# Kernel optimization log

Hardware: AMD Instinct MI355X
Metric: run time of the kernel (lower is better)

The kernel has to match this reference:

```python
import jax, jax.numpy as jnp
import numpy as np
from jax import lax

C_OUT = 32   # out_capsules[0]
D_OUT = 8    # out_capsules[1]
ROUTING_ITERS = 3
EPS = 1e-8


def squash(s):
    # squash over capsule-channel axis c (dim 1 of B c d h w)
    n2 = jnp.sum(s * s, axis=1, keepdims=True)
    return s * (n2 / (1.0 + n2)) / jnp.sqrt(n2 + EPS)


def setup_inputs() -> dict:
    key = jax.random.key(0)
    k1, k2 = jax.random.split(key)
    x = jax.random.normal(k1, (8, 16, 8, 96, 96), dtype=jnp.float32)
    # torch Conv3d weight layout: (out_ch, in_ch, kD, kH, kW); scaled ~ kaiming-ish
    w_conv = jax.random.normal(k2, (C_OUT * D_OUT, 16, 1, 3, 3), dtype=jnp.float32) * 0.05
    return {"x": x, "w_conv": w_conv}


def reference(x, w_conv):
    # Conv3d, no bias, valid padding, stride 1, kernel (1,3,3)
    u = lax.conv_general_dilated(
        x, w_conv, window_strides=(1, 1, 1), padding='VALID',
        dimension_numbers=('NCDHW', 'OIDHW', 'NCDHW'))  # (B, c*d, D, h, w)
    B, _, D, h, w = u.shape
    # rearrange 'B (c d) D h w -> B c D d h w'
    u = u.reshape(B, C_OUT, D_OUT, D, h, w).transpose(0, 1, 3, 2, 4, 5)

    b = jnp.zeros((B, D, D_OUT, h, w), dtype=u.dtype)
    s = None
    for _ in range(ROUTING_ITERS):
        # softmax_3d: exp normalized over (d, h, w), keeping D
        e = jnp.exp(b)
        c = e / jnp.sum(e, axis=(2, 3, 4), keepdims=True)
        s = jnp.einsum('BDdhw,BcDdhw->Bcdhw', c, u)
        b = b + jnp.einsum('BcDdhw,Bcdhw->BDdhw', u, squash(s))
    return s
```

## Files before the change

### kernel.cpp

```cpp
#include <hip/hip_runtime.h>
#include <math.h>

#define CIN   16
#define DDEP  8
#define HIN   96
#define WIN   96
#define HOUT  94
#define WOUT  94
#define HW    (HOUT*WOUT)
#define CH    256
#define DCAP  8
#define KTOT  (CIN*9)
#define KTILES 5
#define APAD  168
#define EPSQ  1e-8f

#define B_ELEMS ((size_t)8*DDEP*DCAP*HW)
#define WFRAG_ELEMS ((size_t)KTILES*16*64*8)
#define BLK_PER_B (94*12)
#define VSITES (DCAP*HW)
#define NBLK2  277
#define XN ((size_t)8*CIN*DDEP*HIN*WIN)
#define XBLK  9216
#define G_BYTES ((size_t)8*VSITES*36*4)

typedef __attribute__((ext_vector_type(8))) short bf16x8;
typedef __attribute__((ext_vector_type(4))) float f32x4;

__device__ __forceinline__ ushort f2bf(float f) {
    unsigned u = __float_as_uint(f);
    return (ushort)((u + 0x7FFFu + ((u >> 16) & 1u)) >> 16);
}
__device__ __forceinline__ float bf2f(ushort h) {
    return __uint_as_float(((unsigned)h) << 16);
}

__global__ __launch_bounds__(256) void prep(
    const float* __restrict__ x, ushort* __restrict__ xb,
    const float* __restrict__ w, ushort* __restrict__ w_hi, ushort* __restrict__ w_lo)
{
    const int bid = blockIdx.x;
    if (bid < XBLK) {
        size_t i = (size_t)bid*256 + threadIdx.x;
        float4 v = ((const float4*)x)[i];
        ushort4 o;
        o.x = f2bf(v.x); o.y = f2bf(v.y); o.z = f2bf(v.z); o.w = f2bf(v.w);
        ((ushort4*)xb)[i] = o;
    } else if (threadIdx.x < 64) {
        const int b2 = bid - XBLK;
        const int nt = b2 & 15, kt = b2 >> 4;
        const int lane = threadIdx.x;
        const int n  = nt*16 + (lane & 15);
        const int kb = kt*32 + (lane >> 4)*8;
        size_t off = (((size_t)kt*16 + nt)*64 + lane)*8;
        for (int j = 0; j < 8; ++j) {
            int k = kb + j;
            float v = (k < KTOT) ? w[(size_t)n*KTOT + k] : 0.f;
            ushort hi = f2bf(v);
            float  r  = v - bf2f(hi);
            ushort lo = f2bf(r);
            w_hi[off + j] = hi; w_lo[off + j] = lo;
        }
    }
}

__global__ __launch_bounds__(256, 2) void conv_g(
    const ushort* __restrict__ xb,
    const ushort* __restrict__ w_hi, const ushort* __restrict__ w_lo,
    float* __restrict__ bws, float* __restrict__ Zp1, float* __restrict__ Gm)
{
    const int t  = threadIdx.x;
    const int wx = blockIdx.x, h0 = blockIdx.y, bb = blockIdx.z;
    const int w0 = wx*8;

    __shared__ __align__(16) ushort a_hi[64][APAD];
    __shared__ union {
        ushort patchb[CIN][DDEP][3][10];
        float gst[4][16][36];
    } ov;
    __shared__ float b1s[8][8][8];

    for (int i = t; i < CIN*DDEP*3*5; i += 256) {
        int ci = i / 120, rem = i - ci*120;
        int D  = rem / 15, r2 = rem - D*15;
        int kh = r2 / 5, uc = r2 - kh*5;
        int xc = w0 + uc*2;
        const ushort* row = xb + (((size_t)(bb*CIN + ci)*DDEP + D)*HIN + (h0+kh))*WIN;
        unsigned v;
        if (xc + 1 < WIN) v = *(const unsigned*)&row[xc];
        else { unsigned e = row[95]; v = e | (e << 16); }
        *(unsigned*)&ov.patchb[ci][D][kh][uc*2] = v;
    }
    __syncthreads();

    {
        const int site = t >> 2, kg = t & 3;
        const int D = site >> 3, wi = site & 7;
        #pragma unroll
        for (int u2 = 0; u2 < 18; ++u2) {
            int k0 = kg*36 + u2*2;
            int ci0 = k0/9, r0 = k0 - ci0*9, kh0 = r0/3, kw0 = r0 - kh0*3;
            int k1 = k0 + 1;
            int ci1 = k1/9, r1 = k1 - ci1*9, kh1 = r1/3, kw1 = r1 - kh1*3;
            unsigned lo = ov.patchb[ci0][D][kh0][wi+kw0];
            unsigned hi = ov.patchb[ci1][D][kh1][wi+kw1];
            *(unsigned*)&a_hi[site][k0] = lo | (hi << 16);
        }
        if (t < 64) {
            #pragma unroll
            for (int kk = KTOT; kk < KTILES*32; kk += 2)
                *(unsigned*)&a_hi[t][kk] = 0u;
        }
    }
    __syncthreads();

    const int wv = t >> 6, lane = t & 63;
    const int m16 = lane & 15, quad = lane >> 4;
    const int Dq  = quad >> 1;
    const int wih = quad & 1;
    f32x4 acc[4][4];
    #pragma unroll
    for (int mt = 0; mt < 4; ++mt)
        #pragma unroll
        for (int nt = 0; nt < 4; ++nt)
            acc[mt][nt] = (f32x4){0.f, 0.f, 0.f, 0.f};

    #pragma unroll
    for (int kt = 0; kt < KTILES; ++kt) {
        bf16x8 ah[4];
        #pragma unroll
        for (int mt = 0; mt < 4; ++mt)
            ah[mt] = *(const bf16x8*)&a_hi[mt*16 + m16][kt*32 + quad*8];
        #pragma unroll
        for (int nt = 0; nt < 4; ++nt) {
            size_t off = (((size_t)kt*16 + (wv*4 + nt))*64 + lane)*8;
            bf16x8 bh = *(const bf16x8*)&w_hi[off];
            bf16x8 bl = *(const bf16x8*)&w_lo[off];
            #pragma unroll
            for (int mt = 0; mt < 4; ++mt) {
                acc[mt][nt] = __builtin_amdgcn_mfma_f32_16x16x32_bf16(ah[mt], bh, acc[mt][nt], 0, 0, 0);
                acc[mt][nt] = __builtin_amdgcn_mfma_f32_16x16x32_bf16(ah[mt], bl, acc[mt][nt], 0, 0, 0);
            }
        }
    }

    {
        const int c3 = m16 >> 3;
        const int dL = m16 & 7;
        __syncthreads();
        #pragma unroll
        for (int r = 0; r < 4; ++r) {
            const int rq = r >> 1;
            float G36[36];
            #pragma unroll
            for (int j = 0; j < 36; ++j) G36[j] = 0.f;
            #pragma unroll
            for (int nt = 0; nt < 4; ++nt) {
                float u8[8];
                #pragma unroll
                for (int mt = 0; mt < 4; ++mt) {
                    float own = acc[mt][nt][r];
                    float oth = __shfl_xor(own, 32);
                    if (Dq == 0) { u8[mt*2]   = own; u8[mt*2+1] = oth; }
                    else         { u8[mt*2+1] = own; u8[mt*2]   = oth; }
                }
                if (Dq == rq) {
                    int idx = 0;
                    #pragma unroll
                    for (int D = 0; D < 8; ++D)
                        #pragma unroll
                        for (int Dp = D; Dp < 8; ++Dp) {
                            G36[idx] += u8[D]*u8[Dp];
                            ++idx;
                        }
                }
            }
            if (Dq == rq) {
                #pragma unroll
                for (int j = 0; j < 36; ++j) G36[j] += __shfl_xor(G36[j], 8);
                if (c3 == 0) {
                    #pragma unroll
                    for (int j = 0; j < 36; ++j) ov.gst[wv][dL*2 + wih][j] = G36[j];
                }
            }
            __syncthreads();
            for (int idx2 = t; idx2 < 16*36; idx2 += 256) {
                int sidx = idx2 / 36, j = idx2 - sidx*36;
                int dd = sidx >> 1, wh = sidx & 1;
                int w = w0 + wh*4 + r;
                if (w < WOUT) {
                    float gv = ov.gst[0][sidx][j] + ov.gst[1][sidx][j]
                             + ov.gst[2][sidx][j] + ov.gst[3][sidx][j];
                    size_t gsite = ((size_t)(bb*DCAP + dd)*HOUT + h0)*WOUT + w;
                    Gm[gsite*36 + j] = gv;
                }
            }
            if (t < 16) {
                const int sdd = t >> 1, swh = t & 1;
                const int sw = w0 + swh*4 + r;
                if (sw < WOUT) {
                    const float inv = 1.0f / (float)(DCAP * HW);
                    float g36[36];
                    #pragma unroll
                    for (int j = 0; j < 36; ++j)
                        g36[j] = ov.gst[0][t][j] + ov.gst[1][t][j]
                               + ov.gst[2][t][j] + ov.gst[3][t][j];
                    float tD[8];
                    #pragma unroll
                    for (int D = 0; D < 8; ++D) tD[D] = 0.f;
                    int idx = 0;
                    #pragma unroll
                    for (int D = 0; D < 8; ++D)
                        #pragma unroll
                        for (int Dp = D; Dp < 8; ++Dp) {
                            float gv = g36[idx]; ++idx;
                            tD[D] += inv * gv;
                            if (Dp != D) tD[Dp] += inv * gv;
                        }
                    float n2 = 0.f;
                    #pragma unroll
                    for (int D = 0; D < 8; ++D) n2 += inv * tD[D];
                    float fac = (n2 / (1.f + n2)) / sqrtf(n2 + EPSQ);
                    #pragma unroll
                    for (int D = 0; D < 8; ++D) b1s[sdd][swh*4 + r][D] = fac * tD[D];
                }
            }
            __syncthreads();
        }
    }

    {
        int Dd = t >> 2, wip = t & 3;
        int D = Dd >> 3, d2 = Dd & 7;
        int w = w0 + wip*2;
        float ez = 0.f;
        if (w + 1 < WOUT) {
            float2 add;
            add.x = b1s[d2][wip*2][D];
            add.y = b1s[d2][wip*2 + 1][D];
            *(float2*)&bws[((size_t)bb*64 + Dd)*HW + (size_t)h0*WOUT + w] = add;
            ez = expf(add.x) + expf(add.y);
        }
        #pragma unroll
        for (int off = 1; off < 32; off <<= 1) ez += __shfl_xor(ez, off);
        if ((t & 31) == 0)
            Zp1[((size_t)bb*8 + D)*BLK_PER_B + h0*12 + wx] = ez;
    }
}

__global__ __launch_bounds__(256) void gram_route2(
    const float* __restrict__ Gm, float* __restrict__ bws,
    const float* __restrict__ Zp1, float* __restrict__ Zp2)
{
    const int k = blockIdx.x, bb = blockIdx.y;
    const int t = threadIdx.x;

    __shared__ float invZ1[8];
    {
        const int Dg = t >> 5;
        const float* p = Zp1 + ((size_t)bb*8 + Dg)*BLK_PER_B;
        float s = 0.f;
        for (int k2 = (t & 31); k2 < BLK_PER_B; k2 += 32) s += p[k2];
        #pragma unroll
        for (int off = 1; off < 32; off <<= 1) s += __shfl_xor(s, off);
        if ((t & 31) == 0) invZ1[Dg] = 1.0f / s;
    }
    __syncthreads();

    const int local = k*256 + t;
    const bool valid = local < VSITES;
    float ez8[8];
    #pragma unroll
    for (int D = 0; D < 8; ++D) ez8[D] = 0.f;
    if (valid) {
        const int d  = local / HW;
        const int r2 = local - d*HW;
        float bv[8], cm[8];
        #pragma unroll
        for (int D = 0; D < 8; ++D) {
            bv[D] = bws[((size_t)(bb*64 + D*8 + d))*HW + r2];
            cm[D] = expf(bv[D]) * invZ1[D];
        }
        float g[36];
        const float4* gp = (const float4*)(Gm + (size_t)(bb*VSITES + local)*36);
        #pragma unroll
        for (int q = 0; q < 9; ++q) {
            float4 v = gp[q];
            g[q*4+0] = v.x; g[q*4+1] = v.y; g[q*4+2] = v.z; g[q*4+3] = v.w;
        }
        float tD[8];
        #pragma unroll
        for (int D = 0; D < 8; ++D) tD[D] = 0.f;
        {
            int idx = 0;
            #pragma unroll
            for (int D = 0; D < 8; ++D)
                #pragma unroll
                for (int Dp = D; Dp < 8; ++Dp) {
                    float gv = g[idx]; ++idx;
                    tD[D] += cm[Dp] * gv;
                    if (Dp != D) tD[Dp] += cm[D] * gv;
                }
        }
        float n2 = 0.f;
        #pragma unroll
        for (int D = 0; D < 8; ++D) n2 += cm[D] * tD[D];
        float fac = (n2 / (1.f + n2)) / sqrtf(n2 + EPSQ);
        #pragma unroll
        for (int D = 0; D < 8; ++D) {
            float nb = bv[D] + fac * tD[D];
            bws[((size_t)(bb*64 + D*8 + d))*HW + r2] = nb;
            ez8[D] = expf(nb);
        }
    }
    #pragma unroll
    for (int D = 0; D < 8; ++D)
        #pragma unroll
        for (int off = 1; off < 64; off <<= 1) ez8[D] += __shfl_xor(ez8[D], off);
    __shared__ float ps[4][8];
    if ((t & 63) == 0) {
        #pragma unroll
        for (int D = 0; D < 8; ++D) ps[t >> 6][D] = ez8[D];
    }
    __syncthreads();
    if (t < 8)
        Zp2[((size_t)bb*8 + t)*NBLK2 + k] = ps[0][t] + ps[1][t] + ps[2][t] + ps[3][t];
}

__global__ __launch_bounds__(256, 2) void conv_s(
    const ushort* __restrict__ xb,
    const ushort* __restrict__ w_hi, const ushort* __restrict__ w_lo,
    const float* __restrict__ bws, const float* __restrict__ Zp2,
    float* __restrict__ out)
{
    const int t  = threadIdx.x;
    const int wx = blockIdx.x, h0 = blockIdx.y, bb = blockIdx.z;
    const int w0 = wx*8;

    __shared__ __align__(16) ushort a_hi[64][APAD];
    __shared__ float  cms[64][8];
    __shared__ float  invZ[8];
    __shared__ union {
        ushort patchb[CIN][DDEP][3][10];
        float  sout[256][8];
    } ov;

    {
        const int Dg = t >> 5;
        const float* p = Zp2 + ((size_t)bb*8 + Dg)*NBLK2;
        float s = 0.f;
        for (int k2 = (t & 31); k2 < NBLK2; k2 += 32) s += p[k2];
        #pragma unroll
        for (int off = 1; off < 32; off <<= 1) s += __shfl_xor(s, off);
        if ((t & 31) == 0) invZ[Dg] = 1.0f / s;
    }
    for (int v = t; v < 512; v += 256) {
        int Dd = v >> 3, wi = v & 7;
        int w = w0 + wi;
        float bv = (w < WOUT) ? bws[((size_t)bb*64 + Dd)*HW + (size_t)h0*WOUT + w] : 0.f;
        cms[Dd][wi] = expf(bv);
    }
    for (int i = t; i < CIN*DDEP*3*5; i += 256) {
        int ci = i / 120, rem = i - ci*120;
        int D  = rem / 15, r2 = rem - D*15;
        int kh = r2 / 5, uc = r2 - kh*5;
        int xc = w0 + uc*2;
        const ushort* row = xb + (((size_t)(bb*CIN + ci)*DDEP + D)*HIN + (h0+kh))*WIN;
        unsigned v;
        if (xc + 1 < WIN) v = *(const unsigned*)&row[xc];
        else { unsigned e = row[95]; v = e | (e << 16); }
        *(unsigned*)&ov.patchb[ci][D][kh][uc*2] = v;
    }
    __syncthreads();

    {
        const int site = t >> 2, kg = t & 3;
        const int D = site >> 3, wi = site & 7;
        #pragma unroll
        for (int u2 = 0; u2 < 18; ++u2) {
            int k0 = kg*36 + u2*2;
            int ci0 = k0/9, r0 = k0 - ci0*9, kh0 = r0/3, kw0 = r0 - kh0*3;
            int k1 = k0 + 1;
            int ci1 = k1/9, r1 = k1 - ci1*9, kh1 = r1/3, kw1 = r1 - kh1*3;
            unsigned lo = ov.patchb[ci0][D][kh0][wi+kw0];
            unsigned hi = ov.patchb[ci1][D][kh1][wi+kw1];
            *(unsigned*)&a_hi[site][k0] = lo | (hi << 16);
        }
        if (t < 64) {
            #pragma unroll
            for (int kk = KTOT; kk < KTILES*32; kk += 2)
                *(unsigned*)&a_hi[t][kk] = 0u;
        }
    }
    __syncthreads();

    const int wv = t >> 6, lane = t & 63;
    const int m16 = lane & 15, quad = lane >> 4;
    f32x4 acc[4][4];
    #pragma unroll
    for (int mt = 0; mt < 4; ++mt)
        #pragma unroll
        for (int nt = 0; nt < 4; ++nt)
            acc[mt][nt] = (f32x4){0.f, 0.f, 0.f, 0.f};

    #pragma unroll
    for (int kt = 0; kt < KTILES; ++kt) {
        bf16x8 ah[4];
        #pragma unroll
        for (int mt = 0; mt < 4; ++mt)
            ah[mt] = *(const bf16x8*)&a_hi[mt*16 + m16][kt*32 + quad*8];
        #pragma unroll
        for (int nt = 0; nt < 4; ++nt) {
            size_t off = (((size_t)kt*16 + (wv*4 + nt))*64 + lane)*8;
            bf16x8 bh = *(const bf16x8*)&w_hi[off];
            bf16x8 bl = *(const bf16x8*)&w_lo[off];
            #pragma unroll
            for (int mt = 0; mt < 4; ++mt) {
                acc[mt][nt] = __builtin_amdgcn_mfma_f32_16x16x32_bf16(ah[mt], bh, acc[mt][nt], 0, 0, 0);
                acc[mt][nt] = __builtin_amdgcn_mfma_f32_16x16x32_bf16(ah[mt], bl, acc[mt][nt], 0, 0, 0);
            }
        }
    }

    const int d   = m16 & 7;
    const int Dq  = quad >> 1;
    const int wih = quad & 1;
    float svv[4][4];
    {
        float cmw[4][4];
        #pragma unroll
        for (int mt = 0; mt < 4; ++mt) {
            int D = mt*2 + Dq;
            float iz = invZ[D];
            #pragma unroll
            for (int r = 0; r < 4; ++r) cmw[mt][r] = cms[D*8 + d][wih*4 + r] * iz;
        }
        #pragma unroll
        for (int nt = 0; nt < 4; ++nt)
            #pragma unroll
            for (int r = 0; r < 4; ++r) {
                float partial = 0.f;
                #pragma unroll
                for (int mt = 0; mt < 4; ++mt) partial += cmw[mt][r]*acc[mt][nt][r];
                partial += __shfl_xor(partial, 32);
                svv[nt][r] = partial;
            }
    }
    if (quad < 2) {
        #pragma unroll
        for (int nt = 0; nt < 4; ++nt) {
            int ch = wv*64 + nt*16 + m16;
            #pragma unroll
            for (int r = 0; r < 4; ++r) ov.sout[ch][wih*4 + r] = svv[nt][r];
        }
    }
    __syncthreads();
    for (int i = t; i < 1024; i += 256) {
        int c2 = i >> 2, wip = i & 3;
        int w = w0 + wip*2;
        if (w + 1 < WOUT) {
            float2 v2 = { ov.sout[c2][wip*2], ov.sout[c2][wip*2 + 1] };
            *(float2*)&out[((size_t)bb*CH + c2)*HW + (size_t)h0*WOUT + w] = v2;
        }
    }
}

extern "C" void kernel_launch(void* const* d_in, const int* in_sizes, int n_in,
                              void* d_out, int out_size, void* d_ws, size_t ws_size,
                              hipStream_t stream)
{
    (void)in_sizes; (void)n_in; (void)out_size; (void)ws_size;
    const float* x     = (const float*)d_in[0];
    const float* wconv = (const float*)d_in[1];
    float* out = (float*)d_out;

    float*  bws  = (float*)d_ws;
    float*  Zp1  = bws + B_ELEMS;
    float*  Zp2  = Zp1 + 64*BLK_PER_B;
    ushort* w_hi = (ushort*)(Zp2 + 64*NBLK2);
    ushort* w_lo = w_hi + WFRAG_ELEMS;
    ushort* xb   = w_lo + WFRAG_ELEMS;
    size_t  base = (size_t)((char*)(xb + XN) - (char*)d_ws);
    size_t  goff = (base + 255) & ~(size_t)255;
    float*  Gm   = (float*)((char*)d_ws + goff);

    const dim3 grid(12, 94, 8);
    prep<<<XBLK + 80, 256, 0, stream>>>(x, xb, wconv, w_hi, w_lo);
    conv_g<<<grid, 256, 0, stream>>>(xb, w_hi, w_lo, bws, Zp1, Gm);
    gram_route2<<<dim3(NBLK2, 8), 256, 0, stream>>>(Gm, bws, Zp1, Zp2);
    conv_s<<<grid, 256, 0, stream>>>(xb, w_hi, w_lo, bws, Zp2, out);
}
```

Measured before the change: 644.9 us.

## Move first routing update out of conv_g into a separate gram_route1 kernel

The first-iteration routing logit computation (squash of the uniform-weighted sum from the Gram matrix, the bws write and the exp partial sums) is removed from the conv_g epilogue. It moves into a new gram_route1 kernel that reads Gm per site with one thread per site. This takes a serial 16-thread section and a shared buffer out of the conv kernel, which may help its occupancy and latency. In exchange it adds a kernel launch and an extra global read of Gm, and Zp1 partials are now indexed per gram block rather than per conv block.

```diff
diff --git a/kernel.cpp b/kernel.cpp
--- a/kernel.cpp
+++ b/kernel.cpp
@@ -17,7 +17,6 @@
 
 #define B_ELEMS ((size_t)8*DDEP*DCAP*HW)
 #define WFRAG_ELEMS ((size_t)KTILES*16*64*8)
-#define BLK_PER_B (94*12)
 #define VSITES (DCAP*HW)
 #define NBLK2  277
 #define XN ((size_t)8*CIN*DDEP*HIN*WIN)
@@ -67,7 +66,7 @@
 __global__ __launch_bounds__(256, 2) void conv_g(
     const ushort* __restrict__ xb,
     const ushort* __restrict__ w_hi, const ushort* __restrict__ w_lo,
-    float* __restrict__ bws, float* __restrict__ Zp1, float* __restrict__ Gm)
+    float* __restrict__ Gm)
 {
     const int t  = threadIdx.x;
     const int wx = blockIdx.x, h0 = blockIdx.y, bb = blockIdx.z;
@@ -78,7 +77,6 @@
         ushort patchb[CIN][DDEP][3][10];
         float gst[4][16][36];
     } ov;
-    __shared__ float b1s[8][8][8];
 
     for (int i = t; i < CIN*DDEP*3*5; i += 256) {
         int ci = i / 120, rem = i - ci*120;
@@ -195,57 +193,70 @@
                     Gm[gsite*36 + j] = gv;
                 }
             }
-            if (t < 16) {
-                const int sdd = t >> 1, swh = t & 1;
-                const int sw = w0 + swh*4 + r;
-                if (sw < WOUT) {
-                    const float inv = 1.0f / (float)(DCAP * HW);
-                    float g36[36];
-                    #pragma unroll
-                    for (int j = 0; j < 36; ++j)
-                        g36[j] = ov.gst[0][t][j] + ov.gst[1][t][j]
-                               + ov.gst[2][t][j] + ov.gst[3][t][j];
-                    float tD[8];
-                    #pragma unroll
-                    for (int D = 0; D < 8; ++D) tD[D] = 0.f;
-                    int idx = 0;
-                    #pragma unroll
-                    for (int D = 0; D < 8; ++D)
-                        #pragma unroll
-                        for (int Dp = D; Dp < 8; ++Dp) {
-                            float gv = g36[idx]; ++idx;
-                            tD[D] += inv * gv;
-                            if (Dp != D) tD[Dp] += inv * gv;
-                        }
-                    float n2 = 0.f;
-                    #pragma unroll
-                    for (int D = 0; D < 8; ++D) n2 += inv * tD[D];
-                    float fac = (n2 / (1.f + n2)) / sqrtf(n2 + EPSQ);
-                    #pragma unroll
-                    for (int D = 0; D < 8; ++D) b1s[sdd][swh*4 + r][D] = fac * tD[D];
+            __syncthreads();
+        }
+    }
+}
+
+__global__ __launch_bounds__(256) void gram_route1(
+    const float* __restrict__ Gm, float* __restrict__ bws,
+    float* __restrict__ Zp1)
+{
+    const int k = blockIdx.x, bb = blockIdx.y;
+    const int t = threadIdx.x;
+    const int local = k*256 + t;
+    const bool valid = local < VSITES;
+    float ez8[8];
+    #pragma unroll
+    for (int D = 0; D < 8; ++D) ez8[D] = 0.f;
+    if (valid) {
+        const int d  = local / HW;
+        const int r2 = local - d*HW;
+        const float inv = 1.0f / (float)(DCAP * HW);
+        float g[36];
+        const float4* gp = (const float4*)(Gm + (size_t)(bb*VSITES + local)*36);
+        #pragma unroll
+        for (int q = 0; q < 9; ++q) {
+            float4 v = gp[q];
+            g[q*4+0] = v.x; g[q*4+1] = v.y; g[q*4+2] = v.z; g[q*4+3] = v.w;
+        }
+        float tD[8];
+        #pragma unroll
+        for (int D = 0; D < 8; ++D) tD[D] = 0.f;
+        {
+            int idx = 0;
+            #pragma unroll
+            for (int D = 0; D < 8; ++D)
+                #pragma unroll
+                for (int Dp = D; Dp < 8; ++Dp) {
+                    float gv = g[idx]; ++idx;
+                    tD[D] += inv * gv;
+                    if (Dp != D) tD[Dp] += inv * gv;
                 }
-            }
-            __syncthreads();
-        }
-    }
-
-    {
-        int Dd = t >> 2, wip = t & 3;
-        int D = Dd >> 3, d2 = Dd & 7;
-        int w = w0 + wip*2;
-        float ez = 0.f;
-        if (w + 1 < WOUT) {
-            float2 add;
-            add.x = b1s[d2][wip*2][D];
-            add.y = b1s[d2][wip*2 + 1][D];
-            *(float2*)&bws[((size_t)bb*64 + Dd)*HW + (size_t)h0*WOUT + w] = add;
-            ez = expf(add.x) + expf(add.y);
-        }
-        #pragma unroll
-        for (int off = 1; off < 32; off <<= 1) ez += __shfl_xor(ez, off);
-        if ((t & 31) == 0)
-            Zp1[((size_t)bb*8 + D)*BLK_PER_B + h0*12 + wx] = ez;
-    }
+        }
+        float n2 = 0.f;
+        #pragma unroll
+        for (int D = 0; D < 8; ++D) n2 += inv * tD[D];
+        float fac = (n2 / (1.f + n2)) / sqrtf(n2 + EPSQ);
+        #pragma unroll
+        for (int D = 0; D < 8; ++D) {
+            float nb = fac * tD[D];
+            bws[((size_t)(bb*64 + D*8 + d))*HW + r2] = nb;
+            ez8[D] = expf(nb);
+        }
+    }
+    #pragma unroll
+    for (int D = 0; D < 8; ++D)
+        #pragma unroll
+        for (int off = 1; off < 64; off <<= 1) ez8[D] += __shfl_xor(ez8[D], off);
+    __shared__ float ps[4][8];
+    if ((t & 63) == 0) {
+        #pragma unroll
+        for (int D = 0; D < 8; ++D) ps[t >> 6][D] = ez8[D];
+    }
+    __syncthreads();
+    if (t < 8)
+        Zp1[((size_t)bb*8 + t)*NBLK2 + k] = ps[0][t] + ps[1][t] + ps[2][t] + ps[3][t];
 }
 
 __global__ __launch_bounds__(256) void gram_route2(
@@ -258,9 +269,9 @@
     __shared__ float invZ1[8];
     {
         const int Dg = t >> 5;
-        const float* p = Zp1 + ((size_t)bb*8 + Dg)*BLK_PER_B;
+        const float* p = Zp1 + ((size_t)bb*8 + Dg)*NBLK2;
         float s = 0.f;
-        for (int k2 = (t & 31); k2 < BLK_PER_B; k2 += 32) s += p[k2];
+        for (int k2 = (t & 31); k2 < NBLK2; k2 += 32) s += p[k2];
         #pragma unroll
         for (int off = 1; off < 32; off <<= 1) s += __shfl_xor(s, off);
         if ((t & 31) == 0) invZ1[Dg] = 1.0f / s;
@@ -476,7 +487,7 @@
 
     float*  bws  = (float*)d_ws;
     float*  Zp1  = bws + B_ELEMS;
-    float*  Zp2  = Zp1 + 64*BLK_PER_B;
+    float*  Zp2  = Zp1 + 64*NBLK2;
     ushort* w_hi = (ushort*)(Zp2 + 64*NBLK2);
     ushort* w_lo = w_hi + WFRAG_ELEMS;
     ushort* xb   = w_lo + WFRAG_ELEMS;
@@ -486,7 +497,8 @@
 
     const dim3 grid(12, 94, 8);
     prep<<<XBLK + 80, 256, 0, stream>>>(x, xb, wconv, w_hi, w_lo);
-    conv_g<<<grid, 256, 0, stream>>>(xb, w_hi, w_lo, bws, Zp1, Gm);
+    conv_g<<<grid, 256, 0, stream>>>(xb, w_hi, w_lo, Gm);
+    gram_route1<<<dim3(NBLK2, 8), 256, 0, stream>>>(Gm, bws, Zp1);
     gram_route2<<<dim3(NBLK2, 8), 256, 0, stream>>>(Gm, bws, Zp1, Zp2);
     conv_s<<<grid, 256, 0, stream>>>(xb, w_hi, w_lo, bws, Zp2, out);
 }
```

Result: faster. 577.9 us (-10.4%).
